# Kernel tuning notes

Hardware: AMD Instinct MI355X
Metric: run time of the kernel (lower is better)

The kernel has to match this reference:

```python
import jax, jax.numpy as jnp
import numpy as np

D = 1024      # model_dim
H = 16        # num_heads
DH = D // H   # depth per head
F = 4096      # ffn_dim
B, L = 4, 2048
LN_EPS = 1e-5


def layer_norm(x, g, b):
    mu = jnp.mean(x, axis=-1, keepdims=True)
    var = jnp.var(x, axis=-1, keepdims=True)
    return (x - mu) * jax.lax.rsqrt(var + LN_EPS) * g + b


def setup_inputs() -> dict:
    key = jax.random.key(0)
    ks = jax.random.split(key, 12)
    s = 0.02
    return {
        "inputs": jax.random.normal(ks[0], (B, L, D), jnp.float32),
        "Wq": jax.random.normal(ks[1], (D, D), jnp.float32) * s,
        "Wk": jax.random.normal(ks[2], (D, D), jnp.float32) * s,
        "Wv": jax.random.normal(ks[3], (D, D), jnp.float32) * s,
        "Wo": jax.random.normal(ks[4], (D, D), jnp.float32) * s,
        "W1": jax.random.normal(ks[5], (F, D), jnp.float32) * s,
        "b1": jnp.zeros((F,), jnp.float32),
        "W2": jax.random.normal(ks[6], (D, F), jnp.float32) * s,
        "b2": jnp.zeros((D,), jnp.float32),
        "ln_g": jnp.ones((D,), jnp.float32),
        "ln_b": jnp.zeros((D,), jnp.float32),
    }


def reference(inputs, Wq, Wk, Wv, Wo, W1, b1, W2, b2, ln_g, ln_b):
    # --- MultiHeadAttention (faithful to source, incl. the bug where
    # ScaledDotProductAttention returns v, not attention @ v) ---
    scale = DH ** -0.5
    q = (inputs @ Wq.T) * scale            # [B,L,D], scaled before head split
    k = inputs @ Wk.T                      # [B,L,D]
    v = inputs @ Wv.T                      # [B,L,D]
    # only the LAST head's attention scores survive the python loop
    qH = q[..., (H - 1) * DH:]             # [B,L,DH]
    kH = k[..., (H - 1) * DH:]             # [B,L,DH]
    attn = jax.nn.softmax(jnp.einsum('bqd,bkd->bqk', qH, kH), axis=-1) / H
    # combine_heads(split_heads(v)) == v, so context = Wo applied to v
    context = v @ Wo.T                     # [B,L,D]; dropout(p=0) is identity

    # --- PositionalWiseFeedForward: conv1d(kernel=1) == pointwise linear ---
    h = jax.nn.relu(context @ W1.T + b1)   # [B,L,F]
    ffn = h @ W2.T + b2                    # [B,L,D]
    out = layer_norm(context + ffn, ln_g, ln_b)
    return out, attn
```

## Files before the change

kernel.cpp:

```cpp
#include <hip/hip_runtime.h>
#include <hip/hip_bf16.h>
#include <stdint.h>

#define D_ 1024
#define H_ 16
#define DH_ 64
#define F_ 4096
#define B_ 4
#define L_ 2048
#define MTOK 8192

typedef __attribute__((ext_vector_type(8))) short bf16x8;
typedef __attribute__((ext_vector_type(4))) float f32x4;

__device__ __forceinline__ short f2bf(float f) {
  uint32_t u = __float_as_uint(f);
  uint32_t r = (u + 0x7FFFu + ((u >> 16) & 1u)) >> 16;
  return (short)(uint16_t)r;
}
__device__ __forceinline__ float bf2f(short s) {
  return __uint_as_float(((uint32_t)(uint16_t)s) << 16);
}

__device__ __forceinline__ void gload_lds16(const short* g, short* l) {
  __builtin_amdgcn_global_load_lds(
      (const __attribute__((address_space(1))) void*)g,
      (__attribute__((address_space(3))) void*)l,
      16, 0, 0);
}

__global__ void __launch_bounds__(256) convert_bf16(
    const float* __restrict__ src, short* __restrict__ dst, long n, float scale) {
  long i = ((long)blockIdx.x * 256 + threadIdx.x) * 4;
  long stride = (long)gridDim.x * 1024;
  for (; i < n; i += stride) {
    float4 f = *(const float4*)(src + i);
    short4 o;
    o.x = f2bf(f.x * scale);
    o.y = f2bf(f.y * scale);
    o.z = f2bf(f.z * scale);
    o.w = f2bf(f.w * scale);
    *(short4*)(dst + i) = o;
  }
}

#define BAR   __builtin_amdgcn_s_barrier()
#define PRIO1 __builtin_amdgcn_s_setprio(1)
#define PRIO0 __builtin_amdgcn_s_setprio(0)
#define LGKM0 asm volatile("s_waitcnt lgkmcnt(0)" ::: "memory")

#define RD_A(mh_, par_) do {                                                  \
  const short* bp = lds + (par_) * BUF + wm * ASLOT;                          \
  _Pragma("unroll")                                                           \
  for (int m2 = 0; m2 < MH; m2++) {                                           \
    const int r = ((mh_) * MH + m2) * 16 + l15;                               \
    _Pragma("unroll")                                                         \
    for (int ks = 0; ks < 2; ks++)                                            \
      aF[mh_][m2][ks] =                                                       \
          *(const bf16x8*)(bp + r * 64 + (((ks * 4 + l4) ^ (r & 7)) << 3));   \
  } } while (0)

#define RD_B(nh_, par_) do {                                                  \
  const short* bp = lds + (par_) * BUF + BM * 64 + (wn >> 1) * 8192;          \
  _Pragma("unroll")                                                           \
  for (int n2 = 0; n2 < 2; n2++) {                                            \
    const int r = (wn & 1) * 64 + ((nh_) * 2 + n2) * 16 + l15;                \
    _Pragma("unroll")                                                         \
    for (int ks = 0; ks < 2; ks++)                                            \
      bF[nh_][n2][ks] =                                                       \
          *(const bf16x8*)(bp + r * 64 + (((ks * 4 + l4) ^ (r & 7)) << 3));   \
  } } while (0)

#define QUAD(mh_, nh_) do {                                                   \
  _Pragma("unroll")                                                           \
  for (int ks = 0; ks < 2; ks++)                                              \
    _Pragma("unroll")                                                         \
    for (int m2 = 0; m2 < MH; m2++)                                           \
      _Pragma("unroll")                                                       \
      for (int n2 = 0; n2 < 2; n2++)                                          \
        acc[(mh_) * MH + m2][(nh_) * 2 + n2] =                                \
            __builtin_amdgcn_mfma_f32_16x16x32_bf16(                          \
                aF[mh_][m2][ks], bF[nh_][n2][ks],                             \
                acc[(mh_) * MH + m2][(nh_) * 2 + n2], 0, 0, 0);               \
} while (0)

#define ITER(g_, SN, SPP, GK) do {                                            \
  const int par = (g_) & 1;                                                   \
                                                                      \
  RD_A(0, par); RD_B(0, par);                                                 \
  if (SN) stA((g_) + 1, 1, par ^ 1);                                          \
  if (BMT == 2) asm volatile("s_waitcnt lgkmcnt(8)" ::: "memory");            \
  BAR; LGKM0;                                                                 \
  PRIO1; QUAD(0, 0); PRIO0;                                                   \
  BAR;                                                                        \
                                                                      \
  RD_B(1, par);                                                               \
  BAR; LGKM0;                                                                 \
  PRIO1; QUAD(0, 1); PRIO0;                                                   \
  BAR;                                                                        \
                                                                      \
  RD_A(1, par);                                                               \
  if (SPP) stB((g_) + 2, 0, par);                                             \
  BAR; LGKM0;                                                                 \
  PRIO1; QUAD(1, 0); PRIO0;                                                   \
  BAR;                                                                        \
                                                                      \
  if (SPP) { stB((g_) + 2, 1, par); stA((g_) + 2, 0, par); }                  \
  PRIO1; QUAD(1, 1); PRIO0;                                                   \
  if (GK == 1) asm volatile("s_waitcnt vmcnt(%0)" :: "i"(VG) : "memory");     \
  else if (GK == 2) asm volatile("s_waitcnt vmcnt(0)" ::: "memory");          \
  BAR;                                                                        \
} while (0)

template<int BMT, bool BIAS, bool RELU>
__global__ void __launch_bounds__(512, 2) gemm8p(
    const short* __restrict__ A, int lda,
    const short* __restrict__ Bm, int ldb,
    short* __restrict__ C, int ldc,
    const float* __restrict__ bias, int K) {
  constexpr int BM = BMT * 128;
  constexpr int MT = BMT * 4;
  constexpr int MH = MT / 2;
  constexpr int LA = BMT;
  constexpr int LB = 2;
  constexpr int ASLOT = (BM / 2) * 64;
  constexpr int BUF = BM * 64 + 16384;
  constexpr int VG = 2 * LB + LA;

  __shared__ __align__(16) short lds[2 * BUF];

  const int tid = threadIdx.x;
  const int lane = tid & 63;
  const int wave = tid >> 6;
  const int wm = wave >> 2, wn = wave & 3;
  const int l15 = lane & 15, l4 = lane >> 4;

  const int id = blockIdx.y * gridDim.x + blockIdx.x;
  const int per = (gridDim.x * gridDim.y) >> 3;
  const int swz = (id & 7) * per + (id >> 3);
  const int bn = swz % gridDim.x;
  const int bm = swz / gridDim.x;

  const short* Ab = A + (long)bm * BM * lda;
  const short* Bb = Bm + (long)bn * 256 * ldb;
  const int NTILE = K >> 6;

  auto stA = [&](int t, int h, int par) {
    short* dst = lds + par * BUF + h * ASLOT;
    const int k0 = t << 6;
#pragma unroll
    for (int l = 0; l < LA; l++) {
      int c = l * 512 + tid;
      int r = c >> 3;
      int cg = (c & 7) ^ (r & 7);
      gload_lds16(Ab + (long)(h * (BM / 2) + r) * lda + k0 + cg * 8, dst + c * 8);
    }
  };
  auto stB = [&](int t, int h, int par) {
    short* dst = lds + par * BUF + BM * 64 + h * 8192;
    const int k0 = t << 6;
#pragma unroll
    for (int l = 0; l < LB; l++) {
      int c = l * 512 + tid;
      int r = c >> 3;
      int cg = (c & 7) ^ (r & 7);
      gload_lds16(Bb + (long)(h * 128 + r) * ldb + k0 + cg * 8, dst + c * 8);
    }
  };

  f32x4 acc[MT][4];
#pragma unroll
  for (int i = 0; i < MT; i++)
#pragma unroll
    for (int j = 0; j < 4; j++) acc[i][j] = (f32x4){0.f, 0.f, 0.f, 0.f};

  bf16x8 aF[2][MH][2];
  bf16x8 bF[2][2][2];

  stA(0, 0, 0); stA(0, 1, 0); stB(0, 0, 0); stB(0, 1, 0);
  stB(1, 0, 1); stB(1, 1, 1); stA(1, 0, 1);
  asm volatile("s_waitcnt vmcnt(%0)" :: "i"(VG) : "memory");
  BAR;

  for (int g = 0; g < NTILE - 2; ++g) ITER(g, 1, 1, 1);
  ITER(NTILE - 2, 1, 0, 2);
  ITER(NTILE - 1, 0, 0, 0);

  const int col0 = bn * 256 + wn * 64;
  const int row0 = bm * BM + wm * (BM / 2);
#pragma unroll
  for (int nt = 0; nt < 4; nt++) {
    const int col = col0 + nt * 16 + l15;
    const float bb = BIAS ? bias[col] : 0.f;
#pragma unroll
    for (int mt = 0; mt < MT; mt++) {
      const int rbase = row0 + mt * 16 + l4 * 4;
#pragma unroll
      for (int r = 0; r < 4; r++) {
        float v = acc[mt][nt][r] + bb;
        if (RELU) v = v > 0.f ? v : 0.f;
        C[(long)(rbase + r) * ldc + col] = f2bf(v);
      }
    }
  }
}

template<bool OUTF32>
__global__ void __launch_bounds__(256) gemm_bt(
    const short* __restrict__ A, int lda, long strideA,
    const short* __restrict__ Bm, int ldb, long strideB,
    void* __restrict__ Cv, int ldc, long strideC, int K) {
  const int bn = blockIdx.x;
  const int bm = blockIdx.y;
  const int bz = blockIdx.z;
  const short* Ab = A + (long)bz * strideA + (long)bm * 128 * lda;
  const short* Bb = Bm + (long)bz * strideB + (long)bn * 128 * ldb;

  __shared__ short lA[128 * 64];
  __shared__ short lB[128 * 64];

  const int tid = threadIdx.x;
  const int lane = tid & 63;
  const int wave = tid >> 6;
  const int wr = wave >> 1, wc = wave & 1;

  f32x4 acc[4][4];
#pragma unroll
  for (int i = 0; i < 4; i++)
#pragma unroll
    for (int j = 0; j < 4; j++) acc[i][j] = (f32x4){0.f, 0.f, 0.f, 0.f};

  for (int k0 = 0; k0 < K; k0 += 64) {
    __syncthreads();
#pragma unroll
    for (int i = 0; i < 4; i++) {
      int c = i * 256 + tid;
      int row = c >> 3;
      int col = (c & 7) * 8;
      gload_lds16(Ab + (long)row * lda + k0 + col, &lA[c * 8]);
      gload_lds16(Bb + (long)row * ldb + k0 + col, &lB[c * 8]);
    }
    __syncthreads();

#pragma unroll
    for (int ks = 0; ks < 2; ks++) {
      bf16x8 af[4], bfr[4];
#pragma unroll
      for (int t = 0; t < 4; t++) {
        af[t]  = *(const bf16x8*)&lA[(wr * 64 + t * 16 + (lane & 15)) * 64 + ks * 32 + (lane >> 4) * 8];
        bfr[t] = *(const bf16x8*)&lB[(wc * 64 + t * 16 + (lane & 15)) * 64 + ks * 32 + (lane >> 4) * 8];
      }
#pragma unroll
      for (int mt = 0; mt < 4; mt++)
#pragma unroll
        for (int nt = 0; nt < 4; nt++)
          acc[mt][nt] = __builtin_amdgcn_mfma_f32_16x16x32_bf16(af[mt], bfr[nt], acc[mt][nt], 0, 0, 0);
    }
  }

  const int col0 = bn * 128 + wc * 64;
  const int row0 = bm * 128 + wr * 64;
#pragma unroll
  for (int mt = 0; mt < 4; mt++) {
#pragma unroll
    for (int nt = 0; nt < 4; nt++) {
      int col = col0 + nt * 16 + (lane & 15);
      int rbase = row0 + mt * 16 + (lane >> 4) * 4;
#pragma unroll
      for (int r = 0; r < 4; r++) {
        float v = acc[mt][nt][r];
        long off = (long)bz * strideC + (long)(rbase + r) * ldc + col;
        if (OUTF32) ((float*)Cv)[off] = v;
        else        ((short*)Cv)[off] = f2bf(v);
      }
    }
  }
}

__device__ __forceinline__ float wave_sum(float v) {
#pragma unroll
  for (int o = 32; o > 0; o >>= 1) v += __shfl_xor(v, o, 64);
  return v;
}
__device__ __forceinline__ float wave_max(float v) {
#pragma unroll
  for (int o = 32; o > 0; o >>= 1) v = fmaxf(v, __shfl_xor(v, o, 64));
  return v;
}

__global__ void __launch_bounds__(256) softmax_div16(float* __restrict__ s) {
  const int tid = threadIdx.x;
  float* p = s + (long)blockIdx.x * 2048;
  float4 a = *(const float4*)(p + tid * 8);
  float4 b = *(const float4*)(p + tid * 8 + 4);
  float m = fmaxf(fmaxf(fmaxf(a.x, a.y), fmaxf(a.z, a.w)),
                  fmaxf(fmaxf(b.x, b.y), fmaxf(b.z, b.w)));
  __shared__ float red[4];
  m = wave_max(m);
  if ((tid & 63) == 0) red[tid >> 6] = m;
  __syncthreads();
  m = fmaxf(fmaxf(red[0], red[1]), fmaxf(red[2], red[3]));

  float e0 = __expf(a.x - m), e1 = __expf(a.y - m), e2 = __expf(a.z - m), e3 = __expf(a.w - m);
  float e4 = __expf(b.x - m), e5 = __expf(b.y - m), e6 = __expf(b.z - m), e7 = __expf(b.w - m);
  float sum = (e0 + e1) + (e2 + e3) + ((e4 + e5) + (e6 + e7));
  __syncthreads();
  sum = wave_sum(sum);
  if ((tid & 63) == 0) red[tid >> 6] = sum;
  __syncthreads();
  sum = red[0] + red[1] + red[2] + red[3];
  float inv = 1.0f / (sum * 16.0f);
  a.x = e0 * inv; a.y = e1 * inv; a.z = e2 * inv; a.w = e3 * inv;
  b.x = e4 * inv; b.y = e5 * inv; b.z = e6 * inv; b.w = e7 * inv;
  *(float4*)(p + tid * 8) = a;
  *(float4*)(p + tid * 8 + 4) = b;
}

__global__ void __launch_bounds__(256) ln_fuse(
    const short* __restrict__ ctx, const short* __restrict__ ffn,
    const float* __restrict__ g, const float* __restrict__ bta,
    float* __restrict__ out) {
  const int tid = threadIdx.x;
  long base = (long)blockIdx.x * 1024 + tid * 4;
  short4 c4 = *(const short4*)(ctx + base);
  short4 f4 = *(const short4*)(ffn + base);
  float x0 = bf2f(c4.x) + bf2f(f4.x);
  float x1 = bf2f(c4.y) + bf2f(f4.y);
  float x2 = bf2f(c4.z) + bf2f(f4.z);
  float x3 = bf2f(c4.w) + bf2f(f4.w);

  float s = (x0 + x1) + (x2 + x3);
  float q = (x0 * x0 + x1 * x1) + (x2 * x2 + x3 * x3);
  __shared__ float rs[4], rq[4];
  s = wave_sum(s);
  q = wave_sum(q);
  if ((tid & 63) == 0) { rs[tid >> 6] = s; rq[tid >> 6] = q; }
  __syncthreads();
  float S = rs[0] + rs[1] + rs[2] + rs[3];
  float Q = rq[0] + rq[1] + rq[2] + rq[3];
  float mu = S * (1.0f / 1024.0f);
  float var = Q * (1.0f / 1024.0f) - mu * mu;
  float inv = rsqrtf(var + 1e-5f);

  float4 g4 = *(const float4*)(g + tid * 4);
  float4 b4 = *(const float4*)(bta + tid * 4);
  float4 o;
  o.x = (x0 - mu) * inv * g4.x + b4.x;
  o.y = (x1 - mu) * inv * g4.y + b4.y;
  o.z = (x2 - mu) * inv * g4.z + b4.z;
  o.w = (x3 - mu) * inv * g4.w + b4.w;
  *(float4*)(out + base) = o;
}

extern "C" void kernel_launch(void* const* d_in, const int* in_sizes, int n_in,
                              void* d_out, int out_size, void* d_ws, size_t ws_size,
                              hipStream_t stream) {
  const float* inputs = (const float*)d_in[0];
  const float* Wq = (const float*)d_in[1];
  const float* Wk = (const float*)d_in[2];
  const float* Wv = (const float*)d_in[3];
  const float* Wo = (const float*)d_in[4];
  const float* W1 = (const float*)d_in[5];
  const float* b1 = (const float*)d_in[6];
  const float* W2 = (const float*)d_in[7];
  const float* b2 = (const float*)d_in[8];
  const float* ln_g = (const float*)d_in[9];
  const float* ln_b = (const float*)d_in[10];

  char* w = (char*)d_ws;
  short* in_bf = (short*)w;  w += (long)MTOK * D_ * 2;
  short* wqk   = (short*)w;  w += 128L * D_ * 2;
  short* wv    = (short*)w;  w += (long)D_ * D_ * 2;
  short* wo    = (short*)w;  w += (long)D_ * D_ * 2;
  short* w1    = (short*)w;  w += (long)F_ * D_ * 2;
  short* w2    = (short*)w;  w += (long)D_ * F_ * 2;
  short* qkh   = (short*)w;  w += (long)MTOK * 128 * 2;
  short* vbf   = (short*)w;  w += (long)MTOK * D_ * 2;
  short* ctxbf = (short*)w;  w += (long)MTOK * D_ * 2;
  short* hbf   = (short*)w;  w += (long)MTOK * F_ * 2;
  short* ffnbf = (short*)w;  w += (long)MTOK * D_ * 2;

  float* out  = (float*)d_out;
  float* attn = out + (long)MTOK * D_;

  const float scale = 0.125f;

  convert_bf16<<<dim3((MTOK * D_) >> 10), 256, 0, stream>>>(inputs, in_bf, (long)MTOK * D_, 1.0f);
  convert_bf16<<<dim3((64 * D_) >> 10), 256, 0, stream>>>(Wq + 960 * D_, wqk, 64L * D_, scale);
  convert_bf16<<<dim3((64 * D_) >> 10), 256, 0, stream>>>(Wk + 960 * D_, wqk + 64L * D_, 64L * D_, 1.0f);
  convert_bf16<<<dim3((D_ * D_) >> 10), 256, 0, stream>>>(Wv, wv, (long)D_ * D_, 1.0f);
  convert_bf16<<<dim3((D_ * D_) >> 10), 256, 0, stream>>>(Wo, wo, (long)D_ * D_, 1.0f);
  convert_bf16<<<dim3((F_ * D_) >> 10), 256, 0, stream>>>(W1, w1, (long)F_ * D_, 1.0f);
  convert_bf16<<<dim3((F_ * D_) >> 10), 256, 0, stream>>>(W2, w2, (long)F_ * D_, 1.0f);

  gemm_bt<false><<<dim3(1, 64, 1), 256, 0, stream>>>(
      in_bf, D_, 0, wqk, D_, 0, qkh, 128, 0, D_);
  gemm8p<1, false, false><<<dim3(4, 64), 512, 0, stream>>>(
      in_bf, D_, wv, D_, vbf, D_, nullptr, D_);
  gemm_bt<true><<<dim3(16, 16, 4), 256, 0, stream>>>(
      qkh, 128, (long)L_ * 128, qkh + 64, 128, (long)L_ * 128,
      attn, L_, (long)L_ * L_, 64);
  softmax_div16<<<dim3(MTOK), 256, 0, stream>>>(attn);
  gemm8p<1, false, false><<<dim3(4, 64), 512, 0, stream>>>(
      vbf, D_, wo, D_, ctxbf, D_, nullptr, D_);
  gemm8p<2, true, true><<<dim3(16, 32), 512, 0, stream>>>(
      ctxbf, D_, w1, D_, hbf, F_, b1, D_);
  gemm8p<1, true, false><<<dim3(4, 64), 512, 0, stream>>>(
      hbf, F_, w2, F_, ffnbf, D_, b2, F_);
  ln_fuse<<<dim3(MTOK), 256, 0, stream>>>(ctxbf, ffnbf, ln_g, ln_b, out);
}
```

Before: 297.9 us.

## Restructure GEMM main loop into two phases with precomputed load addresses

Result: faster. 289.6 us (-2.8%).

```diff
diff --git a/kernel.cpp b/kernel.cpp
--- a/kernel.cpp
+++ b/kernel.cpp
@@ -84,32 +84,22 @@
                 acc[(mh_) * MH + m2][(nh_) * 2 + n2], 0, 0, 0);               \
 } while (0)
 
-#define ITER(g_, SN, SPP, GK) do {                                            \
-  const int par = (g_) & 1;                                                   \
-                                                                      \
-  RD_A(0, par); RD_B(0, par);                                                 \
-  if (SN) stA((g_) + 1, 1, par ^ 1);                                          \
-  if (BMT == 2) asm volatile("s_waitcnt lgkmcnt(8)" ::: "memory");            \
-  BAR; LGKM0;                                                                 \
-  PRIO1; QUAD(0, 0); PRIO0;                                                   \
-  BAR;                                                                        \
-                                                                      \
-  RD_B(1, par);                                                               \
-  BAR; LGKM0;                                                                 \
-  PRIO1; QUAD(0, 1); PRIO0;                                                   \
-  BAR;                                                                        \
-                                                                      \
-  RD_A(1, par);                                                               \
-  if (SPP) stB((g_) + 2, 0, par);                                             \
-  BAR; LGKM0;                                                                 \
-  PRIO1; QUAD(1, 0); PRIO0;                                                   \
-  BAR;                                                                        \
-                                                                      \
-  if (SPP) { stB((g_) + 2, 1, par); stA((g_) + 2, 0, par); }                  \
-  PRIO1; QUAD(1, 1); PRIO0;                                                   \
+#define ITER2(g_, par_, SN, SPP, GK) do {                                     \
+                                                                 \
+  RD_A(0, par_); RD_B(0, par_); RD_B(1, par_);                                \
+  if (SN) stA((g_) + 1, 1, (par_) ^ 1);                                       \
+  LGKM0;                                                                      \
+  PRIO1; QUAD(0, 0); QUAD(0, 1); PRIO0;                                       \
+  BAR;              \
+                                                                 \
+  RD_A(1, par_);                                                              \
+  if (SPP) { stB((g_) + 2, 0, par_); stB((g_) + 2, 1, par_);                  \
+             stA((g_) + 2, 0, par_); }                                        \
+  LGKM0;                                                                      \
+  PRIO1; QUAD(1, 0); QUAD(1, 1); PRIO0;                                       \
   if (GK == 1) asm volatile("s_waitcnt vmcnt(%0)" :: "i"(VG) : "memory");     \
   else if (GK == 2) asm volatile("s_waitcnt vmcnt(0)" ::: "memory");          \
-  BAR;                                                                        \
+  BAR;                          \
 } while (0)
 
 template<int BMT, bool BIAS, bool RELU>
@@ -145,27 +135,32 @@
   const short* Bb = Bm + (long)bn * 256 * ldb;
   const int NTILE = K >> 6;
 
+  const short* gA[2][LA]; short* dA[2][LA];
+  const short* gB[2][LB]; short* dB[2][LB];
+#pragma unroll
+  for (int h = 0; h < 2; h++) {
+#pragma unroll
+    for (int l = 0; l < LA; l++) {
+      int c = l * 512 + tid, r = c >> 3, cg = (c & 7) ^ (r & 7);
+      gA[h][l] = Ab + (long)(h * (BM / 2) + r) * lda + cg * 8;
+      dA[h][l] = lds + h * ASLOT + c * 8;
+    }
+#pragma unroll
+    for (int l = 0; l < LB; l++) {
+      int c = l * 512 + tid, r = c >> 3, cg = (c & 7) ^ (r & 7);
+      gB[h][l] = Bb + (long)(h * 128 + r) * ldb + cg * 8;
+      dB[h][l] = lds + BM * 64 + h * 8192 + c * 8;
+    }
+  }
   auto stA = [&](int t, int h, int par) {
-    short* dst = lds + par * BUF + h * ASLOT;
-    const int k0 = t << 6;
-#pragma unroll
-    for (int l = 0; l < LA; l++) {
-      int c = l * 512 + tid;
-      int r = c >> 3;
-      int cg = (c & 7) ^ (r & 7);
-      gload_lds16(Ab + (long)(h * (BM / 2) + r) * lda + k0 + cg * 8, dst + c * 8);
-    }
+#pragma unroll
+    for (int l = 0; l < LA; l++)
+      gload_lds16(gA[h][l] + (t << 6), dA[h][l] + par * BUF);
   };
   auto stB = [&](int t, int h, int par) {
-    short* dst = lds + par * BUF + BM * 64 + h * 8192;
-    const int k0 = t << 6;
-#pragma unroll
-    for (int l = 0; l < LB; l++) {
-      int c = l * 512 + tid;
-      int r = c >> 3;
-      int cg = (c & 7) ^ (r & 7);
-      gload_lds16(Bb + (long)(h * 128 + r) * ldb + k0 + cg * 8, dst + c * 8);
-    }
+#pragma unroll
+    for (int l = 0; l < LB; l++)
+      gload_lds16(gB[h][l] + (t << 6), dB[h][l] + par * BUF);
   };
 
   f32x4 acc[MT][4];
@@ -182,9 +177,12 @@
   asm volatile("s_waitcnt vmcnt(%0)" :: "i"(VG) : "memory");
   BAR;
 
-  for (int g = 0; g < NTILE - 2; ++g) ITER(g, 1, 1, 1);
-  ITER(NTILE - 2, 1, 0, 2);
-  ITER(NTILE - 1, 0, 0, 0);
+  for (int g = 0; g + 3 < NTILE; g += 2) {
+    ITER2(g, 0, 1, 1, 1);
+    ITER2(g + 1, 1, 1, 1, 1);
+  }
+  ITER2(NTILE - 2, 0, 1, 0, 2);
+  ITER2(NTILE - 1, 1, 0, 0, 0);
 
   const int col0 = bn * 256 + wn * 64;
   const int row0 = bm * BM + wm * (BM / 2);
```
